# Kernel optimization log

Hardware: AMD Instinct MI355X
Metric: run time of the kernel (lower is better)

## Reference

```python
import jax, jax.numpy as jnp
import numpy as np

EMBED = 1024
HEADS = 16
HEAD_DIM = EMBED // HEADS
LN_EPS = 1e-5


def setup_inputs() -> dict:
    key = jax.random.key(0)
    ks = jax.random.split(key, 12)
    B, LQ, LK = 2, 2048, 2048
    s = 1.0 / np.sqrt(EMBED)
    inp = {
        "query_seq": jax.random.normal(ks[0], (B, LQ, EMBED), jnp.float32),
        "key_value_seq": jax.random.normal(ks[1], (B, LK, EMBED), jnp.float32),
        "prompt_size": 0,
        "Wq": jax.random.normal(ks[2], (EMBED, EMBED), jnp.float32) * s,
        "bq": jnp.zeros((EMBED,), jnp.float32),
        "Wk": jax.random.normal(ks[3], (EMBED, EMBED), jnp.float32) * s,
        "bk": jnp.zeros((EMBED,), jnp.float32),
        "Wv": jax.random.normal(ks[4], (EMBED, EMBED), jnp.float32) * s,
        "bv": jnp.zeros((EMBED,), jnp.float32),
        "Wo": jax.random.normal(ks[5], (EMBED, EMBED), jnp.float32) * s,
        "bo": jnp.zeros((EMBED,), jnp.float32),
        "ln_gamma": jnp.ones((EMBED,), jnp.float32),
        "ln_beta": jnp.zeros((EMBED,), jnp.float32),
    }
    return inp


def _split_heads(x):
    B, L, _ = x.shape
    return x.reshape(B, L, HEADS, HEAD_DIM).transpose(0, 2, 1, 3)  # [B,H,L,Dh]


def reference(query_seq, key_value_seq, prompt_size, Wq, bq, Wk, bk, Wv, bv, Wo, bo, ln_gamma, ln_beta):
    # projections (torch nn.Linear: x @ W.T + b)
    q = _split_heads(query_seq @ Wq.T + bq)
    k = _split_heads(key_value_seq @ Wk.T + bk)
    v = _split_heads(key_value_seq @ Wv.T + bv)
    # naive attention: full score matrix, softmax over keys
    scores = jnp.einsum("bhqd,bhkd->bhqk", q, k) / np.sqrt(HEAD_DIM).astype(np.float32)
    attn = jax.nn.softmax(scores, axis=-1)
    ctx = jnp.einsum("bhqk,bhkd->bhqd", attn, v)
    B, H, LQ, Dh = ctx.shape
    ctx = ctx.transpose(0, 2, 1, 3).reshape(B, LQ, H * Dh)
    out = ctx @ Wo.T + bo
    # residual + LayerNorm
    x = out + query_seq
    mu = jnp.mean(x, axis=-1, keepdims=True)
    var = jnp.var(x, axis=-1, keepdims=True)
    return (x - mu) * jax.lax.rsqrt(var + LN_EPS) * ln_gamma + ln_beta
```

## Files before the change

### kernel.cpp

```cpp
#include <hip/hip_runtime.h>

typedef unsigned short u16;
typedef unsigned int u32;
typedef __attribute__((ext_vector_type(8))) __bf16 bf16x8;
typedef __attribute__((ext_vector_type(4))) float f32x4;
typedef __attribute__((ext_vector_type(16))) float f32x16;

#define EMBED 1024
#define NB 2
#define LQ 2048
#define HEADS 16
#define DH 64
#define QSCALE 0.18033688011112042f

__device__ __forceinline__ u16 f2bf(float f) {
  u32 u = __float_as_uint(f);
  u32 r = (u + 0x7FFFu + ((u >> 16) & 1u)) >> 16;
  return (u16)r;
}

__device__ __forceinline__ void glds16(const void* g, void* l) {
  __builtin_amdgcn_global_load_lds((const __attribute__((address_space(1))) void*)g,
                                   (__attribute__((address_space(3))) void*)l, 16, 0, 0);
}

__device__ __forceinline__ f32x4 mfma16(bf16x8 a, bf16x8 b, f32x4 c) {
  return __builtin_amdgcn_mfma_f32_16x16x32_bf16(a, b, c, 0, 0, 0);
}
__device__ __forceinline__ f32x16 mfma32(bf16x8 a, bf16x8 b, f32x16 c) {
  return __builtin_amdgcn_mfma_f32_32x32x16_bf16(a, b, c, 0, 0, 0);
}

__global__ __launch_bounds__(256) void cast_kernel(
    const float* __restrict__ q, const float* __restrict__ kv,
    const float* __restrict__ wq, const float* __restrict__ wk,
    const float* __restrict__ wv, const float* __restrict__ wo,
    u16* __restrict__ qb, u16* __restrict__ kvb, u16* __restrict__ wqb,
    u16* __restrict__ wkb, u16* __restrict__ wvb, u16* __restrict__ wob) {
  int bid = blockIdx.x;
  const float* src;
  u16* dst;
  long base;
  if (bid < 2048) {
    src = q; dst = qb; base = (long)bid * 2048;
  } else if (bid < 4096) {
    src = kv; dst = kvb; base = (long)(bid - 2048) * 2048;
  } else {
    int wsel = (bid - 4096) >> 9;
    int wb = (bid - 4096) & 511;
    if (wsel == 0) { src = wq; dst = wqb; }
    else if (wsel == 1) { src = wk; dst = wkb; }
    else if (wsel == 2) { src = wv; dst = wvb; }
    else { src = wo; dst = wob; }
    base = (long)wb * 2048;
  }
  long e = base + (long)threadIdx.x * 8;
  float4 f0 = *(const float4*)(src + e);
  float4 f1 = *(const float4*)(src + e + 4);
  uint4 o;
  o.x = (u32)f2bf(f0.x) | ((u32)f2bf(f0.y) << 16);
  o.y = (u32)f2bf(f0.z) | ((u32)f2bf(f0.w) << 16);
  o.z = (u32)f2bf(f1.x) | ((u32)f2bf(f1.y) << 16);
  o.w = (u32)f2bf(f1.z) | ((u32)f2bf(f1.w) << 16);
  *(uint4*)(dst + e) = o;
}

template <int IT>
__device__ __forceinline__ void gemm_core(
    u16* As, u16* Bs, const u16* __restrict__ A, const u16* __restrict__ W,
    const float* __restrict__ bias, const float* __restrict__ resid,
    void* __restrict__ outp, int mode, int bx, int by) {
  const int K = EMBED;
  const int TM = IT * 32;
  const int tid = threadIdx.x;
  const int lane = tid & 63;
  const int wv = tid >> 6;
  const int wm = wv >> 1, wn = wv & 1;
  const int l16 = lane & 15, quad = lane >> 4;
  const long tile_m = (long)bx * TM;
  const long tile_n = (long)by * 128;

  f32x4 z4 = {0.f, 0.f, 0.f, 0.f};
  f32x4 acc[IT][4];
#pragma unroll
  for (int i = 0; i < IT; i++)
#pragma unroll
    for (int j = 0; j < 4; j++) acc[i][j] = z4;

  for (int k0 = 0; k0 < K; k0 += 32) {
#pragma unroll
    for (int it = 0; it < TM / 64; it++) {
      int lin = it * 256 + tid;
      int row = lin >> 2, cc = lin & 3;
      glds16(A + (tile_m + row) * K + k0 + ((cc ^ ((row >> 1) & 3)) << 3), As + lin * 8);
    }
#pragma unroll
    for (int it = 0; it < 2; it++) {
      int lin = it * 256 + tid;
      int row = lin >> 2, cc = lin & 3;
      glds16(W + (tile_n + row) * K + k0 + ((cc ^ ((row >> 1) & 3)) << 3), Bs + lin * 8);
    }
    __syncthreads();
    bf16x8 af[IT], bfr[4];
#pragma unroll
    for (int i = 0; i < IT; i++) {
      int row = wm * (IT * 16) + i * 16 + l16;
      af[i] = *(const bf16x8*)(As + row * 32 + ((quad ^ ((row >> 1) & 3)) << 3));
    }
#pragma unroll
    for (int j = 0; j < 4; j++) {
      int row = wn * 64 + j * 16 + l16;
      bfr[j] = *(const bf16x8*)(Bs + row * 32 + ((quad ^ ((row >> 1) & 3)) << 3));
    }
#pragma unroll
    for (int i = 0; i < IT; i++)
#pragma unroll
      for (int j = 0; j < 4; j++) acc[i][j] = mfma16(af[i], bfr[j], acc[i][j]);
    __syncthreads();
  }

#pragma unroll
  for (int j = 0; j < 4; j++) {
    int gn = (int)tile_n + wn * 64 + j * 16 + l16;
    float bv = bias[gn];
#pragma unroll
    for (int i = 0; i < IT; i++) {
#pragma unroll
      for (int r = 0; r < 4; r++) {
        long gm = tile_m + wm * (IT * 16) + i * 16 + quad * 4 + r;
        float v = acc[i][j][r] + bv;
        if (mode == 3) {
          long idx = gm * EMBED + gn;
          ((float*)outp)[idx] = v + resid[idx];
        } else {
          if (mode == 0) v *= QSCALE;
          int b = (int)(gm >> 11), l = (int)(gm & 2047);
          int h = gn >> 6, dh = gn & 63;
          long idx;
          if (mode == 2)
            idx = (long)((b * HEADS + h) * DH + dh) * LQ + l;
          else
            idx = (long)((b * HEADS + h) * LQ + l) * DH + dh;
          ((u16*)outp)[idx] = f2bf(v);
        }
      }
    }
  }
}

__global__ __launch_bounds__(256) void qkv_kernel(
    const u16* __restrict__ qb, const u16* __restrict__ kvb,
    const u16* __restrict__ wqb, const u16* __restrict__ wkb, const u16* __restrict__ wvb,
    const float* __restrict__ bq, const float* __restrict__ bk, const float* __restrict__ bv,
    u16* __restrict__ Qh, u16* __restrict__ Kh, u16* __restrict__ Vt) {
  __shared__ u16 As[128 * 32];
  __shared__ u16 Bs[128 * 32];
  if (blockIdx.z == 0)      gemm_core<4>(As, Bs, qb,  wqb, bq, nullptr, Qh, 0, blockIdx.x, blockIdx.y);
  else if (blockIdx.z == 1) gemm_core<4>(As, Bs, kvb, wkb, bk, nullptr, Kh, 1, blockIdx.x, blockIdx.y);
  else                      gemm_core<4>(As, Bs, kvb, wvb, bv, nullptr, Vt, 2, blockIdx.x, blockIdx.y);
}

__global__ __launch_bounds__(256) void oproj_kernel(
    const u16* __restrict__ ctx, const u16* __restrict__ wob,
    const float* __restrict__ bo, const float* __restrict__ resid, float* __restrict__ out) {
  __shared__ u16 As[64 * 32];
  __shared__ u16 Bs[128 * 32];
  gemm_core<2>(As, Bs, ctx, wob, bo, resid, out, 3, blockIdx.x, blockIdx.y);
}

#define PSTR 72
__global__ __launch_bounds__(256, 2) void attn_kernel(
    const u16* __restrict__ Qh, const u16* __restrict__ Kh,
    const u16* __restrict__ Vt, u16* __restrict__ ctx) {
  __shared__ u16 Qs[128 * 64];
  __shared__ u16 Ks[64 * 64];
  __shared__ u16 Vts[64 * 64];
  __shared__ u16 Pts[128 * PSTR];
  const int tid = threadIdx.x;
  const int lane = tid & 63;
  const int wv = tid >> 6;
  const int l32 = lane & 31, h = lane >> 5;
  const int qt = blockIdx.x, bh = blockIdx.y;
  const long qoff = (long)bh * (LQ * DH) + (long)qt * (128 * DH);
  const long koff = (long)bh * (LQ * DH);
  const long voff = (long)bh * (DH * LQ);
  const int qbase = wv * 32;

#pragma unroll
  for (int it = 0; it < 4; it++) {
    int lin = it * 256 + tid;
    int row = lin >> 3, cc = lin & 7;
    glds16(Qh + qoff + row * 64 + ((cc ^ (row & 7)) << 3), Qs + lin * 8);
  }
  __syncthreads();

  bf16x8 bq[4];
  {
    int row = qbase + l32;
#pragma unroll
    for (int ks = 0; ks < 4; ks++)
      bq[ks] = *(const bf16x8*)(Qs + row * 64 + (((ks * 2 + h) ^ (row & 7)) << 3));
  }

  f32x16 z16 = {0.f, 0.f, 0.f, 0.f, 0.f, 0.f, 0.f, 0.f,
                0.f, 0.f, 0.f, 0.f, 0.f, 0.f, 0.f, 0.f};
  f32x16 ot[2];
  ot[0] = z16;
  ot[1] = z16;
  float lsum = 0.f;
  const int prow = qbase + l32;

  for (int kt = 0; kt < 32; kt++) {
#pragma unroll
    for (int it = 0; it < 2; it++) {
      int lin = it * 256 + tid;
      int row = lin >> 3, cc = lin & 7;
      glds16(Kh + koff + (long)(kt * 64 + row) * 64 + ((cc ^ (row & 7)) << 3), Ks + lin * 8);
    }
#pragma unroll
    for (int it = 0; it < 2; it++) {
      int lin = it * 256 + tid;
      int row = lin >> 3, cc = lin & 7;
      glds16(Vt + voff + (long)row * LQ + kt * 64 + ((cc ^ (row & 7)) << 3), Vts + lin * 8);
    }
    __syncthreads();

    f32x16 st[2];
    st[0] = z16;
    st[1] = z16;
#pragma unroll
    for (int ks = 0; ks < 4; ks++) {
#pragma unroll
      for (int mt = 0; mt < 2; mt++) {
        int row = mt * 32 + l32;
        bf16x8 ak = *(const bf16x8*)(Ks + row * 64 + (((ks * 2 + h) ^ (row & 7)) << 3));
        st[mt] = mfma32(ak, bq[ks], st[mt]);
      }
    }

#pragma unroll
    for (int mt = 0; mt < 2; mt++) {
#pragma unroll
      for (int g = 0; g < 4; g++) {
        float p0 = exp2f(st[mt][g * 4 + 0]);
        float p1 = exp2f(st[mt][g * 4 + 1]);
        float p2 = exp2f(st[mt][g * 4 + 2]);
        float p3 = exp2f(st[mt][g * 4 + 3]);
        lsum += (p0 + p1) + (p2 + p3);
        u32 lo = __builtin_amdgcn_perm(__float_as_uint(p1), __float_as_uint(p0), 0x07060302u);
        u32 hi = __builtin_amdgcn_perm(__float_as_uint(p3), __float_as_uint(p2), 0x07060302u);
        uint2 pk;
        pk.x = lo; pk.y = hi;
        *(uint2*)(Pts + prow * PSTR + mt * 32 + g * 8 + 4 * h) = pk;
      }
    }

#pragma unroll
    for (int ks = 0; ks < 4; ks++) {
      bf16x8 bp = *(const bf16x8*)(Pts + prow * PSTR + ks * 16 + 8 * h);
#pragma unroll
      for (int mt = 0; mt < 2; mt++) {
        int row = mt * 32 + l32;
        bf16x8 av = *(const bf16x8*)(Vts + row * 64 + (((ks * 2 + h) ^ (row & 7)) << 3));
        ot[mt] = mfma32(av, bp, ot[mt]);
      }
    }
    __syncthreads();
  }

  lsum += __shfl_xor(lsum, 32);
  float inv = 1.0f / lsum;

  const int b = bh >> 4, head = bh & 15;
  int qrow = qt * 128 + prow;
  long base = (long)(b * LQ + qrow) * EMBED + head * DH;
#pragma unroll
  for (int mt = 0; mt < 2; mt++) {
#pragma unroll
    for (int g = 0; g < 4; g++) {
      u32 lo = (u32)f2bf(ot[mt][g * 4 + 0] * inv) | ((u32)f2bf(ot[mt][g * 4 + 1] * inv) << 16);
      u32 hi = (u32)f2bf(ot[mt][g * 4 + 2] * inv) | ((u32)f2bf(ot[mt][g * 4 + 3] * inv) << 16);
      uint2 pk;
      pk.x = lo; pk.y = hi;
      *(uint2*)(ctx + base + mt * 32 + g * 8 + 4 * h) = pk;
    }
  }
}

__global__ __launch_bounds__(256) void ln_kernel(
    float* __restrict__ x, const float* __restrict__ gamma, const float* __restrict__ beta) {
  __shared__ float red[8];
  const int tid = threadIdx.x;
  const long row = blockIdx.x;
  float4 v = *(const float4*)(x + row * EMBED + tid * 4);
  float s = v.x + v.y + v.z + v.w;
  float sq = v.x * v.x + v.y * v.y + v.z * v.z + v.w * v.w;
#pragma unroll
  for (int off = 1; off < 64; off <<= 1) {
    s += __shfl_xor(s, off);
    sq += __shfl_xor(sq, off);
  }
  if ((tid & 63) == 0) {
    red[(tid >> 6) * 2] = s;
    red[(tid >> 6) * 2 + 1] = sq;
  }
  __syncthreads();
  s = red[0] + red[2] + red[4] + red[6];
  sq = red[1] + red[3] + red[5] + red[7];
  float mu = s * (1.f / EMBED);
  float var = sq * (1.f / EMBED) - mu * mu;
  float rstd = rsqrtf(var + 1e-5f);
  float4 g = *(const float4*)(gamma + tid * 4);
  float4 bt = *(const float4*)(beta + tid * 4);
  float4 ov;
  ov.x = (v.x - mu) * rstd * g.x + bt.x;
  ov.y = (v.y - mu) * rstd * g.y + bt.y;
  ov.z = (v.z - mu) * rstd * g.z + bt.z;
  ov.w = (v.w - mu) * rstd * g.w + bt.w;
  *(float4*)(x + row * EMBED + tid * 4) = ov;
}

extern "C" void kernel_launch(void* const* d_in, const int* in_sizes, int n_in,
                              void* d_out, int out_size, void* d_ws, size_t ws_size,
                              hipStream_t stream) {
  const float* q     = (const float*)d_in[0];
  const float* kv    = (const float*)d_in[1];
  const float* Wq    = (const float*)d_in[3];
  const float* bq    = (const float*)d_in[4];
  const float* Wk    = (const float*)d_in[5];
  const float* bk    = (const float*)d_in[6];
  const float* Wv    = (const float*)d_in[7];
  const float* bv    = (const float*)d_in[8];
  const float* Wo    = (const float*)d_in[9];
  const float* bo    = (const float*)d_in[10];
  const float* gamma = (const float*)d_in[11];
  const float* beta  = (const float*)d_in[12];

  char* ws = (char*)d_ws;
  u16* qb  = (u16*)(ws + (0l  << 20));
  u16* kvb = (u16*)(ws + (8l  << 20));
  u16* wqb = (u16*)(ws + (16l << 20));
  u16* wkb = (u16*)(ws + (18l << 20));
  u16* wvb = (u16*)(ws + (20l << 20));
  u16* wob = (u16*)(ws + (22l << 20));
  u16* Qh  = (u16*)(ws + (24l << 20));
  u16* Kh  = (u16*)(ws + (32l << 20));
  u16* Vt  = (u16*)(ws + (40l << 20));
  u16* ctx = (u16*)(ws + (48l << 20));
  float* out = (float*)d_out;

  cast_kernel<<<6144, 256, 0, stream>>>(q, kv, Wq, Wk, Wv, Wo, qb, kvb, wqb, wkb, wvb, wob);
  qkv_kernel<<<dim3(32, 8, 3), 256, 0, stream>>>(qb, kvb, wqb, wkb, wvb, bq, bk, bv, Qh, Kh, Vt);
  attn_kernel<<<dim3(16, 32), 256, 0, stream>>>(Qh, Kh, Vt, ctx);
  oproj_kernel<<<dim3(64, 8), 256, 0, stream>>>(ctx, wob, bo, q, out);
  ln_kernel<<<4096, 256, 0, stream>>>(out, gamma, beta);
}
```

Before: 248.1 us.

## Double GEMM K-tile, vectorize V-transposed stores, keep P in registers via lane shuffles

The shared GEMM core now loads 64-wide K slices per iteration with an 8-way XOR swizzle, which halves the number of barrier pairs and doubles the MFMA work per sync. The V-transposed epilogue writes four consecutive bf16 values as one 8-byte store instead of four scattered 2-byte stores. The attention kernel no longer stages the softmax probabilities through shared memory. It builds the MFMA B operand by exchanging packed halves across the two 32-lane halves with shuffles, which frees LDS and drops the 2-blocks launch bound hint. The costs are more shared memory in the GEMMs, higher register pressure, and the possible occupancy change from removing the launch bound.

```diff
diff --git a/kernel.cpp b/kernel.cpp
--- a/kernel.cpp
+++ b/kernel.cpp
@@ -29,6 +29,10 @@
 }
 __device__ __forceinline__ f32x16 mfma32(bf16x8 a, bf16x8 b, f32x16 c) {
   return __builtin_amdgcn_mfma_f32_32x32x16_bf16(a, b, c, 0, 0, 0);
+}
+
+__device__ __forceinline__ u32 packbf(float a, float b) {
+  return __builtin_amdgcn_perm(__float_as_uint(b), __float_as_uint(a), 0x07060302u);
 }
 
 __global__ __launch_bounds__(256) void cast_kernel(
@@ -87,35 +91,41 @@
 #pragma unroll
     for (int j = 0; j < 4; j++) acc[i][j] = z4;
 
-  for (int k0 = 0; k0 < K; k0 += 32) {
-#pragma unroll
-    for (int it = 0; it < TM / 64; it++) {
+  for (int k0 = 0; k0 < K; k0 += 64) {
+#pragma unroll
+    for (int it = 0; it < TM / 32; it++) {
       int lin = it * 256 + tid;
-      int row = lin >> 2, cc = lin & 3;
-      glds16(A + (tile_m + row) * K + k0 + ((cc ^ ((row >> 1) & 3)) << 3), As + lin * 8);
-    }
-#pragma unroll
-    for (int it = 0; it < 2; it++) {
+      int row = lin >> 3, cc = lin & 7;
+      glds16(A + (tile_m + row) * K + k0 + ((cc ^ (row & 7)) << 3), As + lin * 8);
+    }
+#pragma unroll
+    for (int it = 0; it < 4; it++) {
       int lin = it * 256 + tid;
-      int row = lin >> 2, cc = lin & 3;
-      glds16(W + (tile_n + row) * K + k0 + ((cc ^ ((row >> 1) & 3)) << 3), Bs + lin * 8);
+      int row = lin >> 3, cc = lin & 7;
+      glds16(W + (tile_n + row) * K + k0 + ((cc ^ (row & 7)) << 3), Bs + lin * 8);
     }
     __syncthreads();
-    bf16x8 af[IT], bfr[4];
+    bf16x8 af[IT][2], bfr[4][2];
 #pragma unroll
     for (int i = 0; i < IT; i++) {
       int row = wm * (IT * 16) + i * 16 + l16;
-      af[i] = *(const bf16x8*)(As + row * 32 + ((quad ^ ((row >> 1) & 3)) << 3));
+#pragma unroll
+      for (int ki = 0; ki < 2; ki++)
+        af[i][ki] = *(const bf16x8*)(As + row * 64 + (((ki * 4 + quad) ^ (row & 7)) << 3));
     }
 #pragma unroll
     for (int j = 0; j < 4; j++) {
       int row = wn * 64 + j * 16 + l16;
-      bfr[j] = *(const bf16x8*)(Bs + row * 32 + ((quad ^ ((row >> 1) & 3)) << 3));
-    }
-#pragma unroll
-    for (int i = 0; i < IT; i++)
-#pragma unroll
-      for (int j = 0; j < 4; j++) acc[i][j] = mfma16(af[i], bfr[j], acc[i][j]);
+#pragma unroll
+      for (int ki = 0; ki < 2; ki++)
+        bfr[j][ki] = *(const bf16x8*)(Bs + row * 64 + (((ki * 4 + quad) ^ (row & 7)) << 3));
+    }
+#pragma unroll
+    for (int ki = 0; ki < 2; ki++)
+#pragma unroll
+      for (int i = 0; i < IT; i++)
+#pragma unroll
+        for (int j = 0; j < 4; j++) acc[i][j] = mfma16(af[i][ki], bfr[j][ki], acc[i][j]);
     __syncthreads();
   }
 
@@ -125,23 +135,29 @@
     float bv = bias[gn];
 #pragma unroll
     for (int i = 0; i < IT; i++) {
-#pragma unroll
-      for (int r = 0; r < 4; r++) {
-        long gm = tile_m + wm * (IT * 16) + i * 16 + quad * 4 + r;
-        float v = acc[i][j][r] + bv;
-        if (mode == 3) {
-          long idx = gm * EMBED + gn;
-          ((float*)outp)[idx] = v + resid[idx];
-        } else {
+      long gm0 = tile_m + wm * (IT * 16) + i * 16 + quad * 4;
+      if (mode == 3) {
+#pragma unroll
+        for (int r = 0; r < 4; r++) {
+          long idx = (gm0 + r) * EMBED + gn;
+          ((float*)outp)[idx] = acc[i][j][r] + bv + resid[idx];
+        }
+      } else if (mode == 2) {
+        int b = (int)(gm0 >> 11), l = (int)(gm0 & 2047);
+        int hh = gn >> 6, dh = gn & 63;
+        uint2 pk;
+        pk.x = (u32)f2bf(acc[i][j][0] + bv) | ((u32)f2bf(acc[i][j][1] + bv) << 16);
+        pk.y = (u32)f2bf(acc[i][j][2] + bv) | ((u32)f2bf(acc[i][j][3] + bv) << 16);
+        *(uint2*)((u16*)outp + (long)((b * HEADS + hh) * DH + dh) * LQ + l) = pk;
+      } else {
+#pragma unroll
+        for (int r = 0; r < 4; r++) {
+          long gm = gm0 + r;
+          float v = acc[i][j][r] + bv;
           if (mode == 0) v *= QSCALE;
           int b = (int)(gm >> 11), l = (int)(gm & 2047);
-          int h = gn >> 6, dh = gn & 63;
-          long idx;
-          if (mode == 2)
-            idx = (long)((b * HEADS + h) * DH + dh) * LQ + l;
-          else
-            idx = (long)((b * HEADS + h) * LQ + l) * DH + dh;
-          ((u16*)outp)[idx] = f2bf(v);
+          int hh = gn >> 6, dh = gn & 63;
+          ((u16*)outp)[(long)((b * HEADS + hh) * LQ + l) * DH + dh] = f2bf(v);
         }
       }
     }
@@ -153,8 +169,8 @@
     const u16* __restrict__ wqb, const u16* __restrict__ wkb, const u16* __restrict__ wvb,
     const float* __restrict__ bq, const float* __restrict__ bk, const float* __restrict__ bv,
     u16* __restrict__ Qh, u16* __restrict__ Kh, u16* __restrict__ Vt) {
-  __shared__ u16 As[128 * 32];
-  __shared__ u16 Bs[128 * 32];
+  __shared__ u16 As[128 * 64];
+  __shared__ u16 Bs[128 * 64];
   if (blockIdx.z == 0)      gemm_core<4>(As, Bs, qb,  wqb, bq, nullptr, Qh, 0, blockIdx.x, blockIdx.y);
   else if (blockIdx.z == 1) gemm_core<4>(As, Bs, kvb, wkb, bk, nullptr, Kh, 1, blockIdx.x, blockIdx.y);
   else                      gemm_core<4>(As, Bs, kvb, wvb, bv, nullptr, Vt, 2, blockIdx.x, blockIdx.y);
@@ -163,19 +179,17 @@
 __global__ __launch_bounds__(256) void oproj_kernel(
     const u16* __restrict__ ctx, const u16* __restrict__ wob,
     const float* __restrict__ bo, const float* __restrict__ resid, float* __restrict__ out) {
-  __shared__ u16 As[64 * 32];
-  __shared__ u16 Bs[128 * 32];
+  __shared__ u16 As[64 * 64];
+  __shared__ u16 Bs[128 * 64];
   gemm_core<2>(As, Bs, ctx, wob, bo, resid, out, 3, blockIdx.x, blockIdx.y);
 }
 
-#define PSTR 72
-__global__ __launch_bounds__(256, 2) void attn_kernel(
+__global__ __launch_bounds__(256) void attn_kernel(
     const u16* __restrict__ Qh, const u16* __restrict__ Kh,
     const u16* __restrict__ Vt, u16* __restrict__ ctx) {
   __shared__ u16 Qs[128 * 64];
   __shared__ u16 Ks[64 * 64];
   __shared__ u16 Vts[64 * 64];
-  __shared__ u16 Pts[128 * PSTR];
   const int tid = threadIdx.x;
   const int lane = tid & 63;
   const int wv = tid >> 6;
@@ -208,7 +222,6 @@
   ot[0] = z16;
   ot[1] = z16;
   float lsum = 0.f;
-  const int prow = qbase + l32;
 
   for (int kt = 0; kt < 32; kt++) {
 #pragma unroll
@@ -238,6 +251,7 @@
       }
     }
 
+    uint2 pk[2][4];
 #pragma unroll
     for (int mt = 0; mt < 2; mt++) {
 #pragma unroll
@@ -247,22 +261,33 @@
         float p2 = exp2f(st[mt][g * 4 + 2]);
         float p3 = exp2f(st[mt][g * 4 + 3]);
         lsum += (p0 + p1) + (p2 + p3);
-        u32 lo = __builtin_amdgcn_perm(__float_as_uint(p1), __float_as_uint(p0), 0x07060302u);
-        u32 hi = __builtin_amdgcn_perm(__float_as_uint(p3), __float_as_uint(p2), 0x07060302u);
-        uint2 pk;
-        pk.x = lo; pk.y = hi;
-        *(uint2*)(Pts + prow * PSTR + mt * 32 + g * 8 + 4 * h) = pk;
+        pk[mt][g].x = packbf(p0, p1);
+        pk[mt][g].y = packbf(p2, p3);
       }
     }
 
 #pragma unroll
-    for (int ks = 0; ks < 4; ks++) {
-      bf16x8 bp = *(const bf16x8*)(Pts + prow * PSTR + ks * 16 + 8 * h);
-#pragma unroll
-      for (int mt = 0; mt < 2; mt++) {
-        int row = mt * 32 + l32;
-        bf16x8 av = *(const bf16x8*)(Vts + row * 64 + (((ks * 2 + h) ^ (row & 7)) << 3));
-        ot[mt] = mfma32(av, bp, ot[mt]);
+    for (int t = 0; t < 4; t++) {
+      int mt = t >> 1;
+      int s2 = (t & 1) * 2;
+      uint2 own0 = pk[mt][s2], own1 = pk[mt][s2 + 1];
+      uint2 send;
+      send.x = h ? own0.x : own1.x;
+      send.y = h ? own0.y : own1.y;
+      uint2 recv;
+      recv.x = (u32)__shfl_xor((int)send.x, 32);
+      recv.y = (u32)__shfl_xor((int)send.y, 32);
+      uint4 fr;
+      fr.x = h ? recv.x : own0.x;
+      fr.y = h ? recv.y : own0.y;
+      fr.z = h ? own1.x : recv.x;
+      fr.w = h ? own1.y : recv.y;
+      bf16x8 bp = *(bf16x8*)&fr;
+#pragma unroll
+      for (int mt2 = 0; mt2 < 2; mt2++) {
+        int row = mt2 * 32 + l32;
+        bf16x8 av = *(const bf16x8*)(Vts + row * 64 + (((t * 2 + h) ^ (row & 7)) << 3));
+        ot[mt2] = mfma32(av, bp, ot[mt2]);
       }
     }
     __syncthreads();
@@ -272,17 +297,16 @@
   float inv = 1.0f / lsum;
 
   const int b = bh >> 4, head = bh & 15;
-  int qrow = qt * 128 + prow;
+  int qrow = qt * 128 + qbase + l32;
   long base = (long)(b * LQ + qrow) * EMBED + head * DH;
 #pragma unroll
   for (int mt = 0; mt < 2; mt++) {
 #pragma unroll
     for (int g = 0; g < 4; g++) {
-      u32 lo = (u32)f2bf(ot[mt][g * 4 + 0] * inv) | ((u32)f2bf(ot[mt][g * 4 + 1] * inv) << 16);
-      u32 hi = (u32)f2bf(ot[mt][g * 4 + 2] * inv) | ((u32)f2bf(ot[mt][g * 4 + 3] * inv) << 16);
-      uint2 pk;
-      pk.x = lo; pk.y = hi;
-      *(uint2*)(ctx + base + mt * 32 + g * 8 + 4 * h) = pk;
+      uint2 pkk;
+      pkk.x = (u32)f2bf(ot[mt][g * 4 + 0] * inv) | ((u32)f2bf(ot[mt][g * 4 + 1] * inv) << 16);
+      pkk.y = (u32)f2bf(ot[mt][g * 4 + 2] * inv) | ((u32)f2bf(ot[mt][g * 4 + 3] * inv) << 16);
+      *(uint2*)(ctx + base + mt * 32 + g * 8 + 4 * h) = pkk;
     }
   }
 }
```

Result: no change. 251.9 us (+1.6%).
